# Performance work log

Measured on AMD Instinct MI355X. Metric: run time of the kernel, lower is better.

The kernel has to match this reference:

```python
import jax, jax.numpy as jnp
import numpy as np

N, D, V = 4096, 2048, 32000
LSE_SQUARE_SCALE = 1e-4
LABEL_SMOOTHING = 0.1
IGNORE_INDEX = -100
SOFTCAP = 30.0


def setup_inputs() -> dict:
    key = jax.random.key(0)
    k1, k2, k3 = jax.random.split(key, 3)
    return {
        "input": jax.random.normal(k1, (N, D), dtype=jnp.float32),
        "weight": jax.random.normal(k2, (D, V), dtype=jnp.float32),
        "targets": jax.random.randint(k3, (N,), 0, V, dtype=jnp.int64),
        "bias": 0,  # falsy -> no bias branch, matching `if bias:` in the torch module
    }


def reference(input, weight, targets, bias):
    # [N, D] @ [D, V] -> [N, V] logits
    logits = jnp.matmul(input, weight).astype(jnp.float32)
    if bias:
        logits = logits + bias
    # softcap: softcap * tanh(logits / softcap)
    logits = SOFTCAP * jnp.tanh(logits / SOFTCAP)
    logp = jax.nn.log_softmax(logits, axis=-1)          # [N, V]
    lse = logits[:, 0] - logp[:, 0] + 0.0
    lse = jax.scipy.special.logsumexp(logits, axis=-1)  # [N]
    valid = targets != IGNORE_INDEX                     # [N] bool
    safe_t = jnp.where(valid, targets, 0)
    nll = -jnp.take_along_axis(logp, safe_t[:, None], axis=-1)[:, 0]  # [N]
    smooth = -jnp.mean(logp, axis=-1)                   # [N]
    ce_i = (1.0 - LABEL_SMOOTHING) * nll + LABEL_SMOOTHING * smooth
    n_valid = jnp.sum(valid)
    ce_loss = jnp.sum(jnp.where(valid, ce_i, 0.0)) / n_valid
    z_i = jnp.where(valid, LSE_SQUARE_SCALE * lse * lse, 0.0)
    z_loss = jnp.sum(z_i) / n_valid
    return ce_loss + z_loss
```

## Files before the change

kernel.cpp:

```cpp
#include <hip/hip_runtime.h>

#define N_ROWS 4096
#define D_DIM  2048
#define V_DIM  32000

typedef unsigned char u8;
typedef __attribute__((ext_vector_type(2))) long  i64x2;
typedef __attribute__((ext_vector_type(4))) float f32x4;

__device__ __forceinline__ unsigned pack4_fp8(float a, float b, float c, float d) {
    unsigned w = __builtin_amdgcn_cvt_pk_fp8_f32(a, b, 0, false);
    w = __builtin_amdgcn_cvt_pk_fp8_f32(c, d, w, true);
    return w;
}
__device__ __forceinline__ u8 f2fp8(float a) {
    return (u8)(__builtin_amdgcn_cvt_pk_fp8_f32(a, a, 0, false) & 0xFF);
}

__global__ void init_acc(float* __restrict__ p, int n) {
    int i = blockIdx.x * blockDim.x + threadIdx.x;
    if (i < n) p[i] = 0.0f;
}

__global__ void convert_a_fp8(const float4* __restrict__ in, uint4* __restrict__ out,
                              int nchunks) {
    int i = blockIdx.x * blockDim.x + threadIdx.x;
    int stride = gridDim.x * blockDim.x;
    for (; i < nchunks; i += stride) {
        int g = i >> 2, q = i & 3;
        int f4 = g * 16 + q * 2;
        float4 a0 = in[f4],     a1 = in[f4 + 1];
        float4 b0 = in[f4 + 8], b1 = in[f4 + 9];
        uint4 o;
        o.x = pack4_fp8(a0.x, a0.y, a0.z, a0.w);
        o.y = pack4_fp8(a1.x, a1.y, a1.z, a1.w);
        o.z = pack4_fp8(b0.x, b0.y, b0.z, b0.w);
        o.w = pack4_fp8(b1.x, b1.y, b1.z, b1.w);
        out[i] = o;
    }
}

__global__ __launch_bounds__(256) void transpose_w_fp8(const float* __restrict__ W,
                                                       u8* __restrict__ Wt) {
    __shared__ u8 tile[64][72];
    const int v0 = blockIdx.x * 64;
    const int d0 = blockIdx.y * 64;
    const int tid = threadIdx.x;

    const int vch = (tid & 15) * 4;
    const int dr0 = tid >> 4;
#pragma unroll
    for (int i = 0; i < 4; ++i) {
        int d = dr0 + i * 16;
        float4 w = *(const float4*)&W[(size_t)(d0 + d) * V_DIM + v0 + vch];
        tile[vch + 0][d] = f2fp8(w.x);
        tile[vch + 1][d] = f2fp8(w.y);
        tile[vch + 2][d] = f2fp8(w.z);
        tile[vch + 3][d] = f2fp8(w.w);
    }
    __syncthreads();

    const int v = tid >> 2, q = tid & 3;
    uint2 lo = *(const uint2*)&tile[v][q * 8];
    uint2 hi = *(const uint2*)&tile[v][32 + q * 8];
    uint4 o = make_uint4(lo.x, lo.y, hi.x, hi.y);
    *(uint4*)&Wt[(size_t)(v0 + v) * D_DIM + d0 + q * 16] = o;
}

__global__ __launch_bounds__(256) void gemm_ce(
    const u8* __restrict__ A, const u8* __restrict__ Wt,
    const int* __restrict__ targets,
    float* __restrict__ sumexp, float* __restrict__ sumlog, float* __restrict__ tlogit)
{
    __shared__ u8 lsA[128 * 128];
    __shared__ u8 lsB[128 * 128];

    const int tid   = threadIdx.x;
    const int lane  = tid & 63;
    const int wave  = tid >> 6;
    const int wr    = wave >> 1, wc = wave & 1;
    const int col16 = lane & 15, quad = lane >> 4;

    const int rowbase = blockIdx.x * 128;
    const int colbase = blockIdx.y * 128;

    f32x4 acc[4][4];
#pragma unroll
    for (int i = 0; i < 4; ++i)
#pragma unroll
        for (int j = 0; j < 4; ++j)
            acc[i][j] = (f32x4){0.f, 0.f, 0.f, 0.f};

    const int r0   = tid >> 3;
    const int goff = ((tid & 7) ^ (r0 & 7)) * 16;
    const u8* gA = A  + (size_t)(rowbase + r0) * D_DIM + goff;
    const u8* gB = Wt + (size_t)(colbase + r0) * D_DIM + goff;
    u8* lA = &lsA[tid * 16];
    u8* lB = &lsB[tid * 16];

    const int sw    = col16 & 7;
    const int baseA = (wr * 64 + col16) * 128 + ((quad ^ sw) * 16);
    const int baseB = (wc * 64 + col16) * 128 + ((quad ^ sw) * 16);

    for (int kt = 0; kt < D_DIM / 128; ++kt) {
        const int ko = kt * 128;
#pragma unroll
        for (int i = 0; i < 4; ++i) {
            __builtin_amdgcn_global_load_lds(
                (const __attribute__((address_space(1))) void*)(gA + (size_t)i * 32 * D_DIM + ko),
                (__attribute__((address_space(3))) void*)(lA + i * 4096), 16, 0, 0);
            __builtin_amdgcn_global_load_lds(
                (const __attribute__((address_space(1))) void*)(gB + (size_t)i * 32 * D_DIM + ko),
                (__attribute__((address_space(3))) void*)(lB + i * 4096), 16, 0, 0);
        }
        __syncthreads();

        i64x2 aF0[4], aF1[4], bF0[4], bF1[4];
#pragma unroll
        for (int mi = 0; mi < 4; ++mi) {
            aF0[mi] = *(const i64x2*)&lsA[baseA + mi * 2048];
            aF1[mi] = *(const i64x2*)&lsA[(baseA + mi * 2048) ^ 64];
            bF0[mi] = *(const i64x2*)&lsB[baseB + mi * 2048];
            bF1[mi] = *(const i64x2*)&lsB[(baseB + mi * 2048) ^ 64];
        }

#pragma unroll
        for (int mi = 0; mi < 4; ++mi)
#pragma unroll
            for (int ni = 0; ni < 4; ++ni) {
                acc[mi][ni] = __builtin_amdgcn_mfma_f32_16x16x32_fp8_fp8(
                    aF0[mi].x, bF0[ni].x, acc[mi][ni], 0, 0, 0);
                acc[mi][ni] = __builtin_amdgcn_mfma_f32_16x16x32_fp8_fp8(
                    aF0[mi].y, bF0[ni].y, acc[mi][ni], 0, 0, 0);
                acc[mi][ni] = __builtin_amdgcn_mfma_f32_16x16x32_fp8_fp8(
                    aF1[mi].x, bF1[ni].x, acc[mi][ni], 0, 0, 0);
                acc[mi][ni] = __builtin_amdgcn_mfma_f32_16x16x32_fp8_fp8(
                    aF1[mi].y, bF1[ni].y, acc[mi][ni], 0, 0, 0);
            }
        __syncthreads();
    }

#pragma unroll
    for (int mi = 0; mi < 4; ++mi) {
        int grows[4], tgts[4];
#pragma unroll
        for (int r = 0; r < 4; ++r) {
            grows[r] = rowbase + wr * 64 + mi * 16 + quad * 4 + r;
            tgts[r]  = targets[grows[r]];
        }
        float se[4] = {0.f, 0.f, 0.f, 0.f};
        float sl[4] = {0.f, 0.f, 0.f, 0.f};
#pragma unroll
        for (int ni = 0; ni < 4; ++ni) {
            int gcol = colbase + wc * 64 + ni * 16 + col16;
            f32x4 v = acc[mi][ni];
#pragma unroll
            for (int r = 0; r < 4; ++r) {
                float a  = v[r];
                float e2 = __expf(a * (2.0f / 30.0f));
                float th = 1.0f - 2.0f / (e2 + 1.0f);
                float l  = 30.0f * th;
                float el = __expf(l);
                se[r] += el;
                sl[r] += l;
                if (tgts[r] == gcol) tlogit[grows[r]] = l;
            }
        }
#pragma unroll
        for (int r = 0; r < 4; ++r) {
            float e = se[r], s = sl[r];
#pragma unroll
            for (int off = 1; off < 16; off <<= 1) {
                e += __shfl_xor(e, off);
                s += __shfl_xor(s, off);
            }
            if (col16 == 0) {
                atomicAdd(&sumexp[grows[r]], e);
                atomicAdd(&sumlog[grows[r]], s);
            }
        }
    }
}

__global__ void finalize(const float* __restrict__ sumexp, const float* __restrict__ sumlog,
                         const float* __restrict__ tlogit, const int* __restrict__ targets,
                         float* __restrict__ out)
{
    const int tid = threadIdx.x;
    float acc = 0.f, cnt = 0.f;
    for (int r = tid; r < N_ROWS; r += 256) {
        int tg = targets[r];
        if (tg != -100) {
            float lse    = __logf(sumexp[r]);
            float nll    = lse - tlogit[r];
            float smooth = lse - sumlog[r] * (1.0f / V_DIM);
            float ce     = 0.9f * nll + 0.1f * smooth;
            float z      = 1e-4f * lse * lse;
            acc += ce + z;
            cnt += 1.f;
        }
    }
#pragma unroll
    for (int off = 1; off < 64; off <<= 1) {
        acc += __shfl_xor(acc, off);
        cnt += __shfl_xor(cnt, off);
    }
    __shared__ float sa[4], sc[4];
    if ((tid & 63) == 0) { sa[tid >> 6] = acc; sc[tid >> 6] = cnt; }
    __syncthreads();
    if (tid == 0) {
        float t = sa[0] + sa[1] + sa[2] + sa[3];
        float c = sc[0] + sc[1] + sc[2] + sc[3];
        out[0] = t / c;
    }
}

extern "C" void kernel_launch(void* const* d_in, const int* in_sizes, int n_in,
                              void* d_out, int out_size, void* d_ws, size_t ws_size,
                              hipStream_t stream) {
    const float* A  = (const float*)d_in[0];
    const float* W  = (const float*)d_in[1];
    const int*   tg = (const int*)d_in[2];
    float* out = (float*)d_out;

    char* ws = (char*)d_ws;
    u8* A8 = (u8*)ws;
    size_t off = (size_t)N_ROWS * D_DIM;
    u8* Wt8 = (u8*)(ws + off);
    off += (size_t)V_DIM * D_DIM;
    float* sumexp = (float*)(ws + off); off += (size_t)N_ROWS * sizeof(float);
    float* sumlog = (float*)(ws + off); off += (size_t)N_ROWS * sizeof(float);
    float* tlog   = (float*)(ws + off); off += (size_t)N_ROWS * sizeof(float);

    init_acc<<<dim3((N_ROWS * 3 + 255) / 256), 256, 0, stream>>>(sumexp, N_ROWS * 3);
    convert_a_fp8<<<dim3(512), 256, 0, stream>>>((const float4*)A, (uint4*)A8,
                                                 N_ROWS * D_DIM / 16);
    transpose_w_fp8<<<dim3(V_DIM / 64, D_DIM / 64), 256, 0, stream>>>(W, Wt8);
    gemm_ce<<<dim3(N_ROWS / 128, V_DIM / 128), 256, 0, stream>>>(A8, Wt8, tg,
                                                                 sumexp, sumlog, tlog);
    finalize<<<1, 256, 0, stream>>>(sumexp, sumlog, tlog, tg, out);
}
```

Before: 775.8 us.

## Use gfx950 scaled 16x16x128 FP8 MFMA and rework fp8 transpose/convert layouts

Replaces four 16x16x32 FP8 MFMAs per tile with one MFMA-scale 16x16x128 f8f6f4 instruction using unit scales (0x7F exponent). The A and W fp8 layouts are changed to plain contiguous K order, which the wider-K instruction expects, and LDS fragment reads become two 16-byte loads. The W transpose now packs four fp8 values per float4 and transposes 4x4 byte blocks in registers with perm instead of doing byte-wise LDS stores, and the convert grid is enlarged. Correctness depends on the operand K-ordering of the scaled MFMA matching this swizzled layout.

```diff
diff --git a/kernel.cpp b/kernel.cpp
--- a/kernel.cpp
+++ b/kernel.cpp
@@ -5,16 +5,14 @@
 #define V_DIM  32000
 
 typedef unsigned char u8;
-typedef __attribute__((ext_vector_type(2))) long  i64x2;
+typedef __attribute__((ext_vector_type(4))) int   i32x4;
+typedef __attribute__((ext_vector_type(8))) int   i32x8;
 typedef __attribute__((ext_vector_type(4))) float f32x4;
 
 __device__ __forceinline__ unsigned pack4_fp8(float a, float b, float c, float d) {
     unsigned w = __builtin_amdgcn_cvt_pk_fp8_f32(a, b, 0, false);
     w = __builtin_amdgcn_cvt_pk_fp8_f32(c, d, w, true);
     return w;
-}
-__device__ __forceinline__ u8 f2fp8(float a) {
-    return (u8)(__builtin_amdgcn_cvt_pk_fp8_f32(a, a, 0, false) & 0xFF);
 }
 
 __global__ void init_acc(float* __restrict__ p, int n) {
@@ -27,44 +25,53 @@
     int i = blockIdx.x * blockDim.x + threadIdx.x;
     int stride = gridDim.x * blockDim.x;
     for (; i < nchunks; i += stride) {
-        int g = i >> 2, q = i & 3;
-        int f4 = g * 16 + q * 2;
-        float4 a0 = in[f4],     a1 = in[f4 + 1];
-        float4 b0 = in[f4 + 8], b1 = in[f4 + 9];
+        float4 a0 = in[i * 4 + 0], a1 = in[i * 4 + 1];
+        float4 a2 = in[i * 4 + 2], a3 = in[i * 4 + 3];
         uint4 o;
         o.x = pack4_fp8(a0.x, a0.y, a0.z, a0.w);
         o.y = pack4_fp8(a1.x, a1.y, a1.z, a1.w);
-        o.z = pack4_fp8(b0.x, b0.y, b0.z, b0.w);
-        o.w = pack4_fp8(b1.x, b1.y, b1.z, b1.w);
+        o.z = pack4_fp8(a2.x, a2.y, a2.z, a2.w);
+        o.w = pack4_fp8(a3.x, a3.y, a3.z, a3.w);
         out[i] = o;
     }
 }
 
 __global__ __launch_bounds__(256) void transpose_w_fp8(const float* __restrict__ W,
                                                        u8* __restrict__ Wt) {
-    __shared__ u8 tile[64][72];
+    __shared__ alignas(16) unsigned tile[64][20];
+    const int tid = threadIdx.x;
     const int v0 = blockIdx.x * 64;
     const int d0 = blockIdx.y * 64;
-    const int tid = threadIdx.x;
-
     const int vch = (tid & 15) * 4;
-    const int dr0 = tid >> 4;
-#pragma unroll
-    for (int i = 0; i < 4; ++i) {
-        int d = dr0 + i * 16;
-        float4 w = *(const float4*)&W[(size_t)(d0 + d) * V_DIM + v0 + vch];
-        tile[vch + 0][d] = f2fp8(w.x);
-        tile[vch + 1][d] = f2fp8(w.y);
-        tile[vch + 2][d] = f2fp8(w.z);
-        tile[vch + 3][d] = f2fp8(w.w);
-    }
+    const int dgi = tid >> 4;
+
+    unsigned D[4];
+#pragma unroll
+    for (int j = 0; j < 4; ++j) {
+        float4 w = *(const float4*)&W[(size_t)(d0 + dgi * 4 + j) * V_DIM + v0 + vch];
+        D[j] = pack4_fp8(w.x, w.y, w.z, w.w);
+    }
+    unsigned p01l = __builtin_amdgcn_perm(D[1], D[0], 0x05010400u);
+    unsigned p01h = __builtin_amdgcn_perm(D[1], D[0], 0x07030602u);
+    unsigned p23l = __builtin_amdgcn_perm(D[3], D[2], 0x05010400u);
+    unsigned p23h = __builtin_amdgcn_perm(D[3], D[2], 0x07030602u);
+    unsigned o0 = __builtin_amdgcn_perm(p23l, p01l, 0x05040100u);
+    unsigned o1 = __builtin_amdgcn_perm(p23l, p01l, 0x07060302u);
+    unsigned o2 = __builtin_amdgcn_perm(p23h, p01h, 0x05040100u);
+    unsigned o3 = __builtin_amdgcn_perm(p23h, p01h, 0x07060302u);
+
+    const int slot = (dgi >> 2) ^ ((vch >> 2) & 3);
+    const int dpos = slot * 4 + (dgi & 3);
+    tile[vch + 0][dpos] = o0;
+    tile[vch + 1][dpos] = o1;
+    tile[vch + 2][dpos] = o2;
+    tile[vch + 3][dpos] = o3;
     __syncthreads();
 
     const int v = tid >> 2, q = tid & 3;
-    uint2 lo = *(const uint2*)&tile[v][q * 8];
-    uint2 hi = *(const uint2*)&tile[v][32 + q * 8];
-    uint4 o = make_uint4(lo.x, lo.y, hi.x, hi.y);
-    *(uint4*)&Wt[(size_t)(v0 + v) * D_DIM + d0 + q * 16] = o;
+    const int sr = q ^ ((v >> 2) & 3);
+    uint4 val = *(const uint4*)&tile[v][sr * 4];
+    *(uint4*)&Wt[(size_t)(v0 + v) * D_DIM + d0 + q * 16] = val;
 }
 
 __global__ __launch_bounds__(256) void gemm_ce(
@@ -72,8 +79,8 @@
     const int* __restrict__ targets,
     float* __restrict__ sumexp, float* __restrict__ sumlog, float* __restrict__ tlogit)
 {
-    __shared__ u8 lsA[128 * 128];
-    __shared__ u8 lsB[128 * 128];
+    __shared__ alignas(16) u8 lsA[128 * 128];
+    __shared__ alignas(16) u8 lsB[128 * 128];
 
     const int tid   = threadIdx.x;
     const int lane  = tid & 63;
@@ -99,8 +106,8 @@
     u8* lB = &lsB[tid * 16];
 
     const int sw    = col16 & 7;
-    const int baseA = (wr * 64 + col16) * 128 + ((quad ^ sw) * 16);
-    const int baseB = (wc * 64 + col16) * 128 + ((quad ^ sw) * 16);
+    const int baseA = (wr * 64 + col16) * 128 + (((2 * quad) ^ sw) * 16);
+    const int baseB = (wc * 64 + col16) * 128 + (((2 * quad) ^ sw) * 16);
 
     for (int kt = 0; kt < D_DIM / 128; ++kt) {
         const int ko = kt * 128;
@@ -115,28 +122,26 @@
         }
         __syncthreads();
 
-        i64x2 aF0[4], aF1[4], bF0[4], bF1[4];
+        i32x8 aF[4], bF[4];
 #pragma unroll
         for (int mi = 0; mi < 4; ++mi) {
-            aF0[mi] = *(const i64x2*)&lsA[baseA + mi * 2048];
-            aF1[mi] = *(const i64x2*)&lsA[(baseA + mi * 2048) ^ 64];
-            bF0[mi] = *(const i64x2*)&lsB[baseB + mi * 2048];
-            bF1[mi] = *(const i64x2*)&lsB[(baseB + mi * 2048) ^ 64];
+            i32x4 alo = *(const i32x4*)&lsA[baseA + mi * 2048];
+            i32x4 ahi = *(const i32x4*)&lsA[(baseA + mi * 2048) ^ 16];
+            aF[mi] = __builtin_shufflevector(alo, ahi, 0, 1, 2, 3, 4, 5, 6, 7);
+            i32x4 blo = *(const i32x4*)&lsB[baseB + mi * 2048];
+            i32x4 bhi = *(const i32x4*)&lsB[(baseB + mi * 2048) ^ 16];
+            bF[mi] = __builtin_shufflevector(blo, bhi, 0, 1, 2, 3, 4, 5, 6, 7);
         }
 
 #pragma unroll
         for (int mi = 0; mi < 4; ++mi)
 #pragma unroll
-            for (int ni = 0; ni < 4; ++ni) {
-                acc[mi][ni] = __builtin_amdgcn_mfma_f32_16x16x32_fp8_fp8(
-                    aF0[mi].x, bF0[ni].x, acc[mi][ni], 0, 0, 0);
-                acc[mi][ni] = __builtin_amdgcn_mfma_f32_16x16x32_fp8_fp8(
-                    aF0[mi].y, bF0[ni].y, acc[mi][ni], 0, 0, 0);
-                acc[mi][ni] = __builtin_amdgcn_mfma_f32_16x16x32_fp8_fp8(
-                    aF1[mi].x, bF1[ni].x, acc[mi][ni], 0, 0, 0);
-                acc[mi][ni] = __builtin_amdgcn_mfma_f32_16x16x32_fp8_fp8(
-                    aF1[mi].y, bF1[ni].y, acc[mi][ni], 0, 0, 0);
-            }
+            for (int ni = 0; ni < 4; ++ni)
+                acc[mi][ni] = __builtin_amdgcn_mfma_scale_f32_16x16x128_f8f6f4(
+                    aF[mi], bF[ni], acc[mi][ni],
+                    0, 0,
+                    0, 0x7F7F7F7F,
+                    0, 0x7F7F7F7F);
         __syncthreads();
     }
 
@@ -233,8 +238,8 @@
     float* tlog   = (float*)(ws + off); off += (size_t)N_ROWS * sizeof(float);
 
     init_acc<<<dim3((N_ROWS * 3 + 255) / 256), 256, 0, stream>>>(sumexp, N_ROWS * 3);
-    convert_a_fp8<<<dim3(512), 256, 0, stream>>>((const float4*)A, (uint4*)A8,
-                                                 N_ROWS * D_DIM / 16);
+    convert_a_fp8<<<dim3(2048), 256, 0, stream>>>((const float4*)A, (uint4*)A8,
+                                                  N_ROWS * D_DIM / 16);
     transpose_w_fp8<<<dim3(V_DIM / 64, D_DIM / 64), 256, 0, stream>>>(W, Wt8);
     gemm_ce<<<dim3(N_ROWS / 128, V_DIM / 128), 256, 0, stream>>>(A8, Wt8, tg,
                                                                  sumexp, sumlog, tlog);
```

New measurement: 3.051 ms. +293.2%, slower.
